# Kernel tuning notes

Hardware: AMD Instinct MI355X
Metric: run time of the kernel (lower is better)

Reference implementation:

```python
import jax, jax.numpy as jnp
import numpy as np

BSZ, T, D_IN, P, H, D_OUT = 8, 4096, 512, 256, 256, 512


def setup_inputs() -> dict:
    key = jax.random.key(0)
    ks = jax.random.split(key, 8)
    x_seq = jax.random.normal(ks[0], (BSZ, T, D_IN), dtype=jnp.float32)
    # stable diagonal transition: |a| < 1 so the 4096-step recurrence does not blow up
    a = jax.random.uniform(ks[1], (H,), minval=-0.99, maxval=0.99, dtype=jnp.float32)
    B = jax.random.normal(ks[2], (P, H), dtype=jnp.float32) * 0.05
    C = jax.random.normal(ks[3], (H, P), dtype=jnp.float32) * 0.05
    Wi = jax.random.normal(ks[4], (P, D_IN), dtype=jnp.float32) * 0.05
    bi = jax.random.normal(ks[5], (P,), dtype=jnp.float32) * 0.05
    Wo = jax.random.normal(ks[6], (D_OUT, P), dtype=jnp.float32) * 0.05
    bo = jax.random.normal(ks[7], (D_OUT,), dtype=jnp.float32) * 0.05
    return {"x_seq": x_seq, "a": a, "B": B, "C": C, "Wi": Wi, "bi": bi, "Wo": Wo, "bo": bo}


def reference(x_seq, a, B, C, Wi, bi, Wo, bo):
    # proj_in + relu (eqx.nn.Linear: y = W @ x + b), vmapped over batch and time
    x_proj = jax.nn.relu(jnp.einsum("btd,pd->btp", x_seq, Wi) + bi)  # [Bsz,T,P]
    # precompute driving input u_t = B^T x_t for every step
    u = jnp.einsum("btp,ph->bth", x_proj, B)  # [Bsz,T,H]
    u_t = jnp.swapaxes(u, 0, 1)  # [T,Bsz,H] (scan over time)

    def step(h, u_step):  # h: [Bsz,H]
        h = a * h + u_step
        return h, h

    h0 = jnp.zeros((x_seq.shape[0], a.shape[0]), dtype=x_seq.dtype)
    _, hs = jax.lax.scan(step, h0, u_t)  # hs: [T,Bsz,H]
    # y_t = C^T h_t, then proj_out
    y_seq = jnp.einsum("tbh,hp->btp", hs, C)  # [Bsz,T,P]
    y_out = jnp.einsum("btp,op->bto", y_seq, Wo) + bo  # [Bsz,T,D_out]
    return y_out
```

## Files before the change

kernel.cpp:

```cpp
#include <hip/hip_runtime.h>

#define BSZN 8
#define TT 4096
#define DIN 512
#define PP 256
#define HHH 256
#define DOUT 512
#define LCH 64
#define NCH (TT / LCH)
#define NBLK (BSZN * NCH)
#define XPS 264
#define AST 136

typedef __attribute__((ext_vector_type(8))) short bf16x8;
typedef __attribute__((ext_vector_type(4))) float f32x4;

#define GLOBAL_AS __attribute__((address_space(1)))
#define LDS_AS __attribute__((address_space(3)))

static __device__ __forceinline__ void gld_lds16(const void* g, void* l) {
  __builtin_amdgcn_global_load_lds((const GLOBAL_AS unsigned int*)g,
                                   (LDS_AS unsigned int*)l, 16, 0, 0);
}

static __device__ __forceinline__ unsigned short f2bf(float x) {
  union { float f; unsigned u; } t{x};
  unsigned r = t.u + 0x7fffu + ((t.u >> 16) & 1u);
  return (unsigned short)(r >> 16);
}

static __device__ __forceinline__ float ld_carry(const float* p) {
  return __hip_atomic_load(p, __ATOMIC_RELAXED, __HIP_MEMORY_SCOPE_AGENT);
}


__global__ __launch_bounds__(256) void prep_k(
    const float* __restrict__ Wi, const float* __restrict__ Wo,
    const float* __restrict__ Cm, const float* __restrict__ Bm,
    unsigned short* __restrict__ Wi_t, unsigned short* __restrict__ B_t,
    unsigned short* __restrict__ CWT_t, int* __restrict__ flag_g) {
  __shared__ alignas(16) char smem[8192];
  const int b = blockIdx.x, tid = threadIdx.x;
  if (b < 128) {
    const int idx = b * 1024 + tid * 4;
    const int row = idx >> 9, d = idx & 511;
    const float4 v = *(const float4*)(Wi + idx);
    uint2 w;
    w.x = (unsigned)f2bf(v.x) | ((unsigned)f2bf(v.y) << 16);
    w.y = (unsigned)f2bf(v.z) | ((unsigned)f2bf(v.w) << 16);
    const int tile = d >> 5, kc = (d >> 3) & 3, s = (kc + (row >> 1)) & 3;
    *(uint2*)(Wi_t + tile * 8192 + row * 32 + s * 8 + (d & 7)) = w;
  } else if (b < 144) {
    const int t = b - 128;
    const int p0 = (t >> 2) * 64, h0 = (t & 3) * 64;
#pragma unroll 4
    for (int it = 0; it < 16; ++it) {
      const int f = it * 256 + tid;
      const int h = h0 + (f >> 6), p = p0 + (f & 63);
      const unsigned short val = f2bf(Bm[(size_t)p * HHH + h]);
      const int tile = p >> 5, kc = (p >> 3) & 3, s = (kc + (h >> 1)) & 3;
      B_t[tile * 8192 + h * 32 + s * 8 + (p & 7)] = val;
    }
  } else if (b == 144) {
    flag_g[tid] = 0;
    flag_g[tid + 256] = 0;
  } else {
    const int t = b - 145;
    const int m0 = (t >> 2) * 64, n0 = (t & 3) * 64;
    char* As = smem;
    char* Bs = smem + 4096;
    const int wave = tid >> 6, lane = tid & 63;
    const int l15 = lane & 15, q = lane >> 4;
    const int wrow = (wave >> 1) * 32, wcol = (wave & 1) * 32;
    f32x4 acc[2][2];
#pragma unroll
    for (int i = 0; i < 2; ++i)
#pragma unroll
      for (int j = 0; j < 2; ++j) acc[i][j] = f32x4{0.f, 0.f, 0.f, 0.f};
    for (int k0 = 0; k0 < PP; k0 += 32) {
#pragma unroll
      for (int it = 0; it < 2; ++it) {
        const int f = it * 256 + tid;
        const int r = f >> 3, ck = (f & 7) * 4;
        float4 v = *(const float4*)(Wo + (size_t)(m0 + r) * PP + k0 + ck);
        uint2 w;
        w.x = (unsigned)f2bf(v.x) | ((unsigned)f2bf(v.y) << 16);
        w.y = (unsigned)f2bf(v.z) | ((unsigned)f2bf(v.w) << 16);
        *(uint2*)(As + r * 64 + ck * 2) = w;
        v = *(const float4*)(Cm + (size_t)(n0 + r) * PP + k0 + ck);
        w.x = (unsigned)f2bf(v.x) | ((unsigned)f2bf(v.y) << 16);
        w.y = (unsigned)f2bf(v.z) | ((unsigned)f2bf(v.w) << 16);
        *(uint2*)(Bs + r * 64 + ck * 2) = w;
      }
      __syncthreads();
      bf16x8 af[2], bfv[2];
#pragma unroll
      for (int mi = 0; mi < 2; ++mi)
        af[mi] = *(const bf16x8*)(As + (wrow + mi * 16 + l15) * 64 + q * 16);
#pragma unroll
      for (int ni = 0; ni < 2; ++ni)
        bfv[ni] = *(const bf16x8*)(Bs + (wcol + ni * 16 + l15) * 64 + q * 16);
#pragma unroll
      for (int mi = 0; mi < 2; ++mi)
#pragma unroll
        for (int ni = 0; ni < 2; ++ni)
          acc[mi][ni] = __builtin_amdgcn_mfma_f32_16x16x32_bf16(
              af[mi], bfv[ni], acc[mi][ni], 0, 0, 0);
      __syncthreads();
    }
#pragma unroll
    for (int mi = 0; mi < 2; ++mi)
#pragma unroll
      for (int ni = 0; ni < 2; ++ni)
#pragma unroll
        for (int reg = 0; reg < 4; ++reg) {
          const int row = m0 + wrow + mi * 16 + q * 4 + reg;
          const int col = n0 + wcol + ni * 16 + l15;
          const int tile = col >> 5, kc = (col >> 3) & 3;
          const int s = (kc + (row >> 1)) & 3;
          CWT_t[tile * 16384 + row * 32 + s * 8 + (col & 7)] =
              f2bf(acc[mi][ni][reg]);
        }
  }
}

__global__ __launch_bounds__(256, 2) void s4_mega(
    const float* __restrict__ x, const float* __restrict__ a,
    const unsigned short* __restrict__ Wi_t, const float* __restrict__ bi,
    const unsigned short* __restrict__ B_t,
    const unsigned short* __restrict__ CWT_t, const float* __restrict__ bo,
    float* __restrict__ out, float* __restrict__ carry_g,
    int* __restrict__ flag_g) {
  __shared__ alignas(16) char smem[67584];
  char* As = smem;
  unsigned short* xp = (unsigned short*)smem;
  char* TB0 = smem + 33792;
  char* TB1 = smem + 50176;
  float* PL = (float*)(smem + 66560);

  const int tid = threadIdx.x, wave = tid >> 6, lane = tid & 63;
  const int l15 = lane & 15, q = lane >> 4;
  const int bc = blockIdx.x, b = bc >> 6, c = bc & (NCH - 1);
  const size_t row0 = (size_t)bc * LCH;
  const int wc = wave * 64;

  int wrot[4];
#pragma unroll
  for (int ni = 0; ni < 4; ++ni) {
    const int r = wc + ni * 16 + l15;
    wrot[ni] = r * 64 + (((q + (r >> 1)) & 3) << 4);
  }
  int afb[4];
#pragma unroll
  for (int mi = 0; mi < 4; ++mi) afb[mi] = (mi * 16 + l15) * AST + q * 16;
  int xpb[4];
#pragma unroll
  for (int mi = 0; mi < 4; ++mi) xpb[mi] = (mi * 16 + l15) * XPS + q * 8;

  f32x4 acc[4][4];
#pragma unroll
  for (int i = 0; i < 4; ++i)
#pragma unroll
    for (int j = 0; j < 4; ++j) acc[i][j] = f32x4{0.f, 0.f, 0.f, 0.f};

  float4 xv[4];
#pragma unroll
  for (int i = 0; i < 4; ++i) {
    const int f = i * 256 + tid;
    xv[i] = *(const float4*)(x + (row0 + (f >> 4)) * DIN + (f & 15) * 4);
  }
  for (int t = 0; t < 8; ++t) {
    {
#pragma unroll
      for (int i = 0; i < 4; ++i) {
        const int f = i * 256 + tid;
        uint2 w;
        w.x = (unsigned)f2bf(xv[i].x) | ((unsigned)f2bf(xv[i].y) << 16);
        w.y = (unsigned)f2bf(xv[i].z) | ((unsigned)f2bf(xv[i].w) << 16);
        *(uint2*)(As + (f >> 4) * AST + (f & 15) * 8) = w;
      }
    }
    {
      const char* gw = (const char*)Wi_t + t * 32768 + wave * 4096 + lane * 16;
      char* l0 = TB0 + wave * 4096 + lane * 16;
      char* l1 = TB1 + wave * 4096 + lane * 16;
#pragma unroll
      for (int i = 0; i < 4; ++i) {
        gld_lds16(gw + i * 1024, l0 + i * 1024);
        gld_lds16(gw + 16384 + i * 1024, l1 + i * 1024);
      }
    }
    __syncthreads();
    if (t < 7) {
#pragma unroll
      for (int i = 0; i < 4; ++i) {
        const int f = i * 256 + tid;
        xv[i] = *(const float4*)(x + (row0 + (f >> 4)) * DIN + (t + 1) * 64 +
                                 (f & 15) * 4);
      }
    }
    bf16x8 af[4][2], bfv[4][2];
#pragma unroll
    for (int mi = 0; mi < 4; ++mi) {
      af[mi][0] = *(const bf16x8*)(As + afb[mi]);
      af[mi][1] = *(const bf16x8*)(As + afb[mi] + 64);
    }
#pragma unroll
    for (int ni = 0; ni < 4; ++ni) {
      bfv[ni][0] = *(const bf16x8*)(TB0 + wrot[ni]);
      bfv[ni][1] = *(const bf16x8*)(TB1 + wrot[ni]);
    }
#pragma unroll
    for (int kk = 0; kk < 2; ++kk)
#pragma unroll
      for (int mi = 0; mi < 4; ++mi)
#pragma unroll
        for (int ni = 0; ni < 4; ++ni)
          acc[mi][ni] = __builtin_amdgcn_mfma_f32_16x16x32_bf16(
              af[mi][kk], bfv[ni][kk], acc[mi][ni], 0, 0, 0);
    __syncthreads();
  }

#pragma unroll
  for (int ni = 0; ni < 4; ++ni) {
    const int col = wc + ni * 16 + l15;
    const float bb = bi[col];
#pragma unroll
    for (int mi = 0; mi < 4; ++mi)
#pragma unroll
      for (int reg = 0; reg < 4; ++reg) {
        const int row = mi * 16 + q * 4 + reg;
        xp[row * XPS + col] = f2bf(fmaxf(acc[mi][ni][reg] + bb, 0.f));
      }
  }
  __syncthreads();

#pragma unroll
  for (int i = 0; i < 4; ++i)
#pragma unroll
    for (int j = 0; j < 4; ++j) acc[i][j] = f32x4{0.f, 0.f, 0.f, 0.f};
  for (int t = 0; t < 4; ++t) {
    {
      const char* gw = (const char*)B_t + t * 32768 + wave * 4096 + lane * 16;
      char* l0 = TB0 + wave * 4096 + lane * 16;
      char* l1 = TB1 + wave * 4096 + lane * 16;
#pragma unroll
      for (int i = 0; i < 4; ++i) {
        gld_lds16(gw + i * 1024, l0 + i * 1024);
        gld_lds16(gw + 16384 + i * 1024, l1 + i * 1024);
      }
    }
    __syncthreads();
    bf16x8 af[4][2], bfv[4][2];
#pragma unroll
    for (int mi = 0; mi < 4; ++mi) {
      af[mi][0] = *(const bf16x8*)(xp + xpb[mi] + t * 64);
      af[mi][1] = *(const bf16x8*)(xp + xpb[mi] + t * 64 + 32);
    }
#pragma unroll
    for (int ni = 0; ni < 4; ++ni) {
      bfv[ni][0] = *(const bf16x8*)(TB0 + wrot[ni]);
      bfv[ni][1] = *(const bf16x8*)(TB1 + wrot[ni]);
    }
#pragma unroll
    for (int kk = 0; kk < 2; ++kk)
#pragma unroll
      for (int mi = 0; mi < 4; ++mi)
#pragma unroll
        for (int ni = 0; ni < 4; ++ni)
          acc[mi][ni] = __builtin_amdgcn_mfma_f32_16x16x32_bf16(
              af[mi][kk], bfv[ni][kk], acc[mi][ni], 0, 0, 0);
    __syncthreads();
  }

  float aC[4], Wz[4];
#pragma unroll
  for (int ni = 0; ni < 4; ++ni) aC[ni] = a[wc + ni * 16 + l15];
#pragma unroll
  for (int ni = 0; ni < 4; ++ni) {
    const float A = aC[ni];
    const float A2 = A * A, A4 = A2 * A2, A8 = A4 * A4, A16 = A8 * A8;
    const float A4q = ((q & 1) ? A4 : 1.f) * ((q & 2) ? A8 : 1.f);
    float W = 0.f;
#pragma unroll
    for (int mi = 0; mi < 4; ++mi) {
      f32x4 v = acc[mi][ni];
      v.y = fmaf(A, v.x, v.y);
      v.z = fmaf(A, v.y, v.z);
      v.w = fmaf(A, v.z, v.w);
      const float E = v.w;
      const float E0 = __shfl(E, l15, 64);
      const float E1 = __shfl(E, l15 + 16, 64);
      const float E2 = __shfl(E, l15 + 32, 64);
      const float E3 = __shfl(E, l15 + 48, 64);
      const float s1 = E0, s2 = fmaf(A4, s1, E1), s3 = fmaf(A4, s2, E2);
      const float s4 = fmaf(A4, s3, E3);
      const float Sq = (q == 0) ? 0.f : (q == 1) ? s1 : (q == 2) ? s2 : s3;
      const float sin_ = fmaf(A4q, W, Sq);
      v.x = fmaf(A, sin_, v.x);
      v.y = fmaf(A2, sin_, v.y);
      v.z = fmaf(A2 * A, sin_, v.z);
      v.w = fmaf(A4, sin_, v.w);
      acc[mi][ni] = v;
      W = fmaf(A16, W, s4);
    }
    Wz[ni] = W;
  }
  if (q == 0) {
#pragma unroll
    for (int ni = 0; ni < 4; ++ni)
      __hip_atomic_store(&carry_g[(size_t)bc * HHH + wc + ni * 16 + l15],
                         Wz[ni], __ATOMIC_RELAXED, __HIP_MEMORY_SCOPE_AGENT);
  }
  __syncthreads();
  if (tid == 0) {
    __threadfence();
    __hip_atomic_store(&flag_g[bc], 1, __ATOMIC_RELEASE,
                       __HIP_MEMORY_SCOPE_AGENT);
  }
  if (tid < c) {
    while (__hip_atomic_load(&flag_g[b * NCH + tid], __ATOMIC_ACQUIRE,
                             __HIP_MEMORY_SCOPE_AGENT) == 0)
      __builtin_amdgcn_s_sleep(8);
  }
  __syncthreads();
  {
    const int colp = tid;
    const float A = a[colp];
    float t1 = A;
#pragma unroll
    for (int j = 0; j < 6; ++j) t1 *= t1;
    const float A64 = t1, A128 = A64 * A64, A256 = A128 * A128;
    const float* cg = carry_g + (size_t)b * NCH * HHH + colp;
    float P = 0.f;
    int j = 0;
    for (; j + 4 <= c; j += 4) {
      const float c0 = ld_carry(cg + (size_t)j * HHH);
      const float c1 = ld_carry(cg + (size_t)(j + 1) * HHH);
      const float c2 = ld_carry(cg + (size_t)(j + 2) * HHH);
      const float c3 = ld_carry(cg + (size_t)(j + 3) * HHH);
      P = fmaf(A256, P, fmaf(A64, fmaf(A64, fmaf(A64, c0, c1), c2), c3));
    }
    for (; j < c; ++j) P = fmaf(A64, P, ld_carry(cg + (size_t)j * HHH));
    PL[colp] = P;
  }
  __syncthreads();
#pragma unroll
  for (int ni = 0; ni < 4; ++ni) {
    const float A = aC[ni];
    const float A2 = A * A, A4 = A2 * A2, A8 = A4 * A4, A16 = A8 * A8;
    const float A4q = ((q & 1) ? A4 : 1.f) * ((q & 2) ? A8 : 1.f);
    const float P = PL[wc + ni * 16 + l15];
    float fm = A4q * A * P;
#pragma unroll
    for (int mi = 0; mi < 4; ++mi) {
      f32x4 v = acc[mi][ni];
      v.x += fm;
      v.y = fmaf(A, fm, v.y);
      v.z = fmaf(A2, fm, v.z);
      v.w = fmaf(A2 * A, fm, v.w);
      acc[mi][ni] = v;
      fm *= A16;
    }
  }
  __syncthreads();

  unsigned short* hsL = (unsigned short*)smem;
#pragma unroll
  for (int ni = 0; ni < 4; ++ni) {
    const int col = wc + ni * 16 + l15;
#pragma unroll
    for (int mi = 0; mi < 4; ++mi)
#pragma unroll
      for (int reg = 0; reg < 4; ++reg)
        hsL[(mi * 16 + q * 4 + reg) * XPS + col] = f2bf(acc[mi][ni][reg]);
  }
  __syncthreads();

  int crot[2][4];
#pragma unroll
  for (int g = 0; g < 2; ++g)
#pragma unroll
    for (int ni = 0; ni < 4; ++ni) {
      const int r = wave * 128 + g * 64 + ni * 16 + l15;
      crot[g][ni] = r * 64 + (((q + (r >> 1)) & 3) << 4);
    }

  f32x4 oacc[2][4][4];
#pragma unroll
  for (int g = 0; g < 2; ++g)
#pragma unroll
    for (int i = 0; i < 4; ++i)
#pragma unroll
      for (int j = 0; j < 4; ++j) oacc[g][i][j] = f32x4{0.f, 0.f, 0.f, 0.f};
  for (int t = 0; t < 8; ++t) {
    {
      const char* gw =
          (const char*)CWT_t + t * 32768 + wave * 8192 + lane * 16;
      char* l0 = TB0 + wave * 8192 + lane * 16;
#pragma unroll
      for (int i = 0; i < 8; ++i) gld_lds16(gw + i * 1024, l0 + i * 1024);
    }
    __syncthreads();
    bf16x8 af[4], bfv[2][4];
#pragma unroll
    for (int mi = 0; mi < 4; ++mi)
      af[mi] = *(const bf16x8*)(hsL + xpb[mi] + t * 32);
#pragma unroll
    for (int g = 0; g < 2; ++g)
#pragma unroll
      for (int ni = 0; ni < 4; ++ni)
        bfv[g][ni] = *(const bf16x8*)(TB0 + crot[g][ni]);
#pragma unroll
    for (int g = 0; g < 2; ++g)
#pragma unroll
      for (int mi = 0; mi < 4; ++mi)
#pragma unroll
        for (int ni = 0; ni < 4; ++ni)
          oacc[g][mi][ni] = __builtin_amdgcn_mfma_f32_16x16x32_bf16(
              af[mi], bfv[g][ni], oacc[g][mi][ni], 0, 0, 0);
    __syncthreads();
  }
#pragma unroll
  for (int g = 0; g < 2; ++g)
#pragma unroll
    for (int ni = 0; ni < 4; ++ni) {
      const int ocol = wave * 128 + g * 64 + ni * 16 + l15;
      const float bb = bo[ocol];
#pragma unroll
      for (int mi = 0; mi < 4; ++mi)
#pragma unroll
        for (int reg = 0; reg < 4; ++reg) {
          const int row = mi * 16 + q * 4 + reg;
          out[(row0 + row) * DOUT + ocol] = oacc[g][mi][ni][reg] + bb;
        }
    }
}

extern "C" void kernel_launch(void* const* d_in, const int* in_sizes, int n_in,
                              void* d_out, int out_size, void* d_ws,
                              size_t ws_size, hipStream_t stream) {
  const float* x  = (const float*)d_in[0];
  const float* a  = (const float*)d_in[1];
  const float* Bm = (const float*)d_in[2];
  const float* Cm = (const float*)d_in[3];
  const float* Wi = (const float*)d_in[4];
  const float* bi = (const float*)d_in[5];
  const float* Wo = (const float*)d_in[6];
  const float* bo = (const float*)d_in[7];
  float* out = (float*)d_out;

  char* ws = (char*)d_ws;
  unsigned short* Wi_t  = (unsigned short*)ws; ws += (size_t)PP * DIN * 2;
  unsigned short* B_t   = (unsigned short*)ws; ws += (size_t)HHH * PP * 2;
  unsigned short* CWT_t = (unsigned short*)ws; ws += (size_t)DOUT * HHH * 2;
  float* carry_g = (float*)ws; ws += (size_t)NBLK * HHH * 4;
  int* flag_g = (int*)ws;

  prep_k<<<177, 256, 0, stream>>>(Wi, Wo, Cm, Bm, Wi_t, B_t, CWT_t, flag_g);
  s4_mega<<<NBLK, 256, 0, stream>>>(x, a, Wi_t, bi, B_t, CWT_t, bo, out,
                                    carry_g, flag_g);
}
```

Before: 188.7 us.

## Unfuse C and Wo into separate GEMMs and prefetch weight tiles early

The precomputed C·Wo product is dropped, so the prep kernel no longer runs a small GEMM and only converts and lays out B, C and Wo in parallel blocks. The main kernel now does an extra 64x256x256 GEMM with C before the Wo projection. The first weight tile of each stage is issued before the preceding epilogue to overlap its load, and a few barriers are removed. The carry-prefix loop is unrolled by 8 and the spin sleep is lengthened. This shortens the prep stage and hides load latency, at the cost of extra MFMA work per block and an extra bf16 rounding of the intermediate.

```diff
diff --git a/kernel.cpp b/kernel.cpp
--- a/kernel.cpp
+++ b/kernel.cpp
@@ -38,8 +38,8 @@
     const float* __restrict__ Wi, const float* __restrict__ Wo,
     const float* __restrict__ Cm, const float* __restrict__ Bm,
     unsigned short* __restrict__ Wi_t, unsigned short* __restrict__ B_t,
-    unsigned short* __restrict__ CWT_t, int* __restrict__ flag_g) {
-  __shared__ alignas(16) char smem[8192];
+    unsigned short* __restrict__ C_t, unsigned short* __restrict__ Wo_t,
+    int* __restrict__ flag_g) {
   const int b = blockIdx.x, tid = threadIdx.x;
   if (b < 128) {
     const int idx = b * 1024 + tid * 4;
@@ -50,77 +50,40 @@
     w.y = (unsigned)f2bf(v.z) | ((unsigned)f2bf(v.w) << 16);
     const int tile = d >> 5, kc = (d >> 3) & 3, s = (kc + (row >> 1)) & 3;
     *(uint2*)(Wi_t + tile * 8192 + row * 32 + s * 8 + (d & 7)) = w;
-  } else if (b < 144) {
-    const int t = b - 128;
-    const int p0 = (t >> 2) * 64, h0 = (t & 3) * 64;
-#pragma unroll 4
-    for (int it = 0; it < 16; ++it) {
-      const int f = it * 256 + tid;
-      const int h = h0 + (f >> 6), p = p0 + (f & 63);
-      const unsigned short val = f2bf(Bm[(size_t)p * HHH + h]);
-      const int tile = p >> 5, kc = (p >> 3) & 3, s = (kc + (h >> 1)) & 3;
-      B_t[tile * 8192 + h * 32 + s * 8 + (p & 7)] = val;
-    }
-  } else if (b == 144) {
+  } else if (b < 192) {
+    const int f = (b - 128) * 256 + tid;
+    const int p = f >> 6, h = (f & 63) * 4;
+    const float4 v = *(const float4*)(Bm + (size_t)p * HHH + h);
+    const float vv[4] = {v.x, v.y, v.z, v.w};
+    const int tile = p >> 5, kc = (p >> 3) & 3;
+#pragma unroll
+    for (int j = 0; j < 4; ++j) {
+      const int row = h + j, s = (kc + (row >> 1)) & 3;
+      B_t[tile * 8192 + row * 32 + s * 8 + (p & 7)] = f2bf(vv[j]);
+    }
+  } else if (b < 256) {
+    const int f = (b - 192) * 256 + tid;
+    const int h = f >> 6, p = (f & 63) * 4;
+    const float4 v = *(const float4*)(Cm + (size_t)h * PP + p);
+    const float vv[4] = {v.x, v.y, v.z, v.w};
+    const int tile = h >> 5, kc = (h >> 3) & 3;
+#pragma unroll
+    for (int j = 0; j < 4; ++j) {
+      const int row = p + j, s = (kc + (row >> 1)) & 3;
+      C_t[tile * 8192 + row * 32 + s * 8 + (h & 7)] = f2bf(vv[j]);
+    }
+  } else if (b < 384) {
+    const int idx = (b - 256) * 1024 + tid * 4;
+    const int o = idx >> 8, p = idx & 255;
+    const float4 v = *(const float4*)(Wo + idx);
+    uint2 w;
+    w.x = (unsigned)f2bf(v.x) | ((unsigned)f2bf(v.y) << 16);
+    w.y = (unsigned)f2bf(v.z) | ((unsigned)f2bf(v.w) << 16);
+    const int tile = p >> 5, kc = (p >> 3) & 3, s = (kc + (o >> 1)) & 3;
+    *(uint2*)(Wo_t + tile * 16384 + o * 32 + s * 8 + (p & 7)) = w;
+  } else {
     flag_g[tid] = 0;
     flag_g[tid + 256] = 0;
-  } else {
-    const int t = b - 145;
-    const int m0 = (t >> 2) * 64, n0 = (t & 3) * 64;
-    char* As = smem;
-    char* Bs = smem + 4096;
-    const int wave = tid >> 6, lane = tid & 63;
-    const int l15 = lane & 15, q = lane >> 4;
-    const int wrow = (wave >> 1) * 32, wcol = (wave & 1) * 32;
-    f32x4 acc[2][2];
-#pragma unroll
-    for (int i = 0; i < 2; ++i)
-#pragma unroll
-      for (int j = 0; j < 2; ++j) acc[i][j] = f32x4{0.f, 0.f, 0.f, 0.f};
-    for (int k0 = 0; k0 < PP; k0 += 32) {
-#pragma unroll
-      for (int it = 0; it < 2; ++it) {
-        const int f = it * 256 + tid;
-        const int r = f >> 3, ck = (f & 7) * 4;
-        float4 v = *(const float4*)(Wo + (size_t)(m0 + r) * PP + k0 + ck);
-        uint2 w;
-        w.x = (unsigned)f2bf(v.x) | ((unsigned)f2bf(v.y) << 16);
-        w.y = (unsigned)f2bf(v.z) | ((unsigned)f2bf(v.w) << 16);
-        *(uint2*)(As + r * 64 + ck * 2) = w;
-        v = *(const float4*)(Cm + (size_t)(n0 + r) * PP + k0 + ck);
-        w.x = (unsigned)f2bf(v.x) | ((unsigned)f2bf(v.y) << 16);
-        w.y = (unsigned)f2bf(v.z) | ((unsigned)f2bf(v.w) << 16);
-        *(uint2*)(Bs + r * 64 + ck * 2) = w;
-      }
-      __syncthreads();
-      bf16x8 af[2], bfv[2];
-#pragma unroll
-      for (int mi = 0; mi < 2; ++mi)
-        af[mi] = *(const bf16x8*)(As + (wrow + mi * 16 + l15) * 64 + q * 16);
-#pragma unroll
-      for (int ni = 0; ni < 2; ++ni)
-        bfv[ni] = *(const bf16x8*)(Bs + (wcol + ni * 16 + l15) * 64 + q * 16);
-#pragma unroll
-      for (int mi = 0; mi < 2; ++mi)
-#pragma unroll
-        for (int ni = 0; ni < 2; ++ni)
-          acc[mi][ni] = __builtin_amdgcn_mfma_f32_16x16x32_bf16(
-              af[mi], bfv[ni], acc[mi][ni], 0, 0, 0);
-      __syncthreads();
-    }
-#pragma unroll
-    for (int mi = 0; mi < 2; ++mi)
-#pragma unroll
-      for (int ni = 0; ni < 2; ++ni)
-#pragma unroll
-        for (int reg = 0; reg < 4; ++reg) {
-          const int row = m0 + wrow + mi * 16 + q * 4 + reg;
-          const int col = n0 + wcol + ni * 16 + l15;
-          const int tile = col >> 5, kc = (col >> 3) & 3;
-          const int s = (kc + (row >> 1)) & 3;
-          CWT_t[tile * 16384 + row * 32 + s * 8 + (col & 7)] =
-              f2bf(acc[mi][ni][reg]);
-        }
   }
 }
 
@@ -128,14 +91,14 @@
     const float* __restrict__ x, const float* __restrict__ a,
     const unsigned short* __restrict__ Wi_t, const float* __restrict__ bi,
     const unsigned short* __restrict__ B_t,
-    const unsigned short* __restrict__ CWT_t, const float* __restrict__ bo,
+    const unsigned short* __restrict__ C_t,
+    const unsigned short* __restrict__ Wo_t, const float* __restrict__ bo,
     float* __restrict__ out, float* __restrict__ carry_g,
     int* __restrict__ flag_g) {
   __shared__ alignas(16) char smem[67584];
   char* As = smem;
   unsigned short* xp = (unsigned short*)smem;
-  char* TB0 = smem + 33792;
-  char* TB1 = smem + 50176;
+  char* TB = smem + 33792;
   float* PL = (float*)(smem + 66560);
 
   const int tid = threadIdx.x, wave = tid >> 6, lane = tid & 63;
@@ -150,12 +113,22 @@
     const int r = wc + ni * 16 + l15;
     wrot[ni] = r * 64 + (((q + (r >> 1)) & 3) << 4);
   }
+  int crot[2][4];
+#pragma unroll
+  for (int g = 0; g < 2; ++g)
+#pragma unroll
+    for (int ni = 0; ni < 4; ++ni) {
+      const int r = wave * 128 + g * 64 + ni * 16 + l15;
+      crot[g][ni] = r * 64 + (((q + (r >> 1)) & 3) << 4);
+    }
   int afb[4];
 #pragma unroll
   for (int mi = 0; mi < 4; ++mi) afb[mi] = (mi * 16 + l15) * AST + q * 16;
   int xpb[4];
 #pragma unroll
   for (int mi = 0; mi < 4; ++mi) xpb[mi] = (mi * 16 + l15) * XPS + q * 8;
+
+  const int sbase = wave * 4096 + lane * 16;
 
   f32x4 acc[4][4];
 #pragma unroll
@@ -170,24 +143,20 @@
     xv[i] = *(const float4*)(x + (row0 + (f >> 4)) * DIN + (f & 15) * 4);
   }
   for (int t = 0; t < 8; ++t) {
+#pragma unroll
+    for (int i = 0; i < 4; ++i) {
+      const int f = i * 256 + tid;
+      uint2 w;
+      w.x = (unsigned)f2bf(xv[i].x) | ((unsigned)f2bf(xv[i].y) << 16);
+      w.y = (unsigned)f2bf(xv[i].z) | ((unsigned)f2bf(xv[i].w) << 16);
+      *(uint2*)(As + (f >> 4) * AST + (f & 15) * 8) = w;
+    }
     {
+      const char* gw = (const char*)Wi_t + t * 32768 + sbase;
 #pragma unroll
       for (int i = 0; i < 4; ++i) {
-        const int f = i * 256 + tid;
-        uint2 w;
-        w.x = (unsigned)f2bf(xv[i].x) | ((unsigned)f2bf(xv[i].y) << 16);
-        w.y = (unsigned)f2bf(xv[i].z) | ((unsigned)f2bf(xv[i].w) << 16);
-        *(uint2*)(As + (f >> 4) * AST + (f & 15) * 8) = w;
-      }
-    }
-    {
-      const char* gw = (const char*)Wi_t + t * 32768 + wave * 4096 + lane * 16;
-      char* l0 = TB0 + wave * 4096 + lane * 16;
-      char* l1 = TB1 + wave * 4096 + lane * 16;
-#pragma unroll
-      for (int i = 0; i < 4; ++i) {
-        gld_lds16(gw + i * 1024, l0 + i * 1024);
-        gld_lds16(gw + 16384 + i * 1024, l1 + i * 1024);
+        gld_lds16(gw + i * 1024, TB + sbase + i * 1024);
+        gld_lds16(gw + 16384 + i * 1024, TB + 16384 + sbase + i * 1024);
       }
     }
     __syncthreads();
@@ -207,8 +176,8 @@
     }
 #pragma unroll
     for (int ni = 0; ni < 4; ++ni) {
-      bfv[ni][0] = *(const bf16x8*)(TB0 + wrot[ni]);
-      bfv[ni][1] = *(const bf16x8*)(TB1 + wrot[ni]);
+      bfv[ni][0] = *(const bf16x8*)(TB + wrot[ni]);
+      bfv[ni][1] = *(const bf16x8*)(TB + 16384 + wrot[ni]);
     }
 #pragma unroll
     for (int kk = 0; kk < 2; ++kk)
@@ -219,6 +188,15 @@
           acc[mi][ni] = __builtin_amdgcn_mfma_f32_16x16x32_bf16(
               af[mi][kk], bfv[ni][kk], acc[mi][ni], 0, 0, 0);
     __syncthreads();
+  }
+
+  {
+    const char* gw = (const char*)B_t + sbase;
+#pragma unroll
+    for (int i = 0; i < 4; ++i) {
+      gld_lds16(gw + i * 1024, TB + sbase + i * 1024);
+      gld_lds16(gw + 16384 + i * 1024, TB + 16384 + sbase + i * 1024);
+    }
   }
 
 #pragma unroll
@@ -233,21 +211,18 @@
         xp[row * XPS + col] = f2bf(fmaxf(acc[mi][ni][reg] + bb, 0.f));
       }
   }
-  __syncthreads();
 
 #pragma unroll
   for (int i = 0; i < 4; ++i)
 #pragma unroll
     for (int j = 0; j < 4; ++j) acc[i][j] = f32x4{0.f, 0.f, 0.f, 0.f};
   for (int t = 0; t < 4; ++t) {
-    {
-      const char* gw = (const char*)B_t + t * 32768 + wave * 4096 + lane * 16;
-      char* l0 = TB0 + wave * 4096 + lane * 16;
-      char* l1 = TB1 + wave * 4096 + lane * 16;
+    if (t > 0) {
+      const char* gw = (const char*)B_t + t * 32768 + sbase;
 #pragma unroll
       for (int i = 0; i < 4; ++i) {
-        gld_lds16(gw + i * 1024, l0 + i * 1024);
-        gld_lds16(gw + 16384 + i * 1024, l1 + i * 1024);
+        gld_lds16(gw + i * 1024, TB + sbase + i * 1024);
+        gld_lds16(gw + 16384 + i * 1024, TB + 16384 + sbase + i * 1024);
       }
     }
     __syncthreads();
@@ -259,8 +234,8 @@
     }
 #pragma unroll
     for (int ni = 0; ni < 4; ++ni) {
-      bfv[ni][0] = *(const bf16x8*)(TB0 + wrot[ni]);
-      bfv[ni][1] = *(const bf16x8*)(TB1 + wrot[ni]);
+      bfv[ni][0] = *(const bf16x8*)(TB + wrot[ni]);
+      bfv[ni][1] = *(const bf16x8*)(TB + 16384 + wrot[ni]);
     }
 #pragma unroll
     for (int kk = 0; kk < 2; ++kk)
@@ -318,10 +293,18 @@
     __hip_atomic_store(&flag_g[bc], 1, __ATOMIC_RELEASE,
                        __HIP_MEMORY_SCOPE_AGENT);
   }
+  {
+    const char* gw = (const char*)C_t + sbase;
+#pragma unroll
+    for (int i = 0; i < 4; ++i) {
+      gld_lds16(gw + i * 1024, TB + sbase + i * 1024);
+      gld_lds16(gw + 16384 + i * 1024, TB + 16384 + sbase + i * 1024);
+    }
+  }
   if (tid < c) {
     while (__hip_atomic_load(&flag_g[b * NCH + tid], __ATOMIC_ACQUIRE,
                              __HIP_MEMORY_SCOPE_AGENT) == 0)
-      __builtin_amdgcn_s_sleep(8);
+      __builtin_amdgcn_s_sleep(32);
   }
   __syncthreads();
   {
@@ -331,15 +314,18 @@
 #pragma unroll
     for (int j = 0; j < 6; ++j) t1 *= t1;
     const float A64 = t1, A128 = A64 * A64, A256 = A128 * A128;
+    const float A512 = A256 * A256;
     const float* cg = carry_g + (size_t)b * NCH * HHH + colp;
     float P = 0.f;
     int j = 0;
-    for (; j + 4 <= c; j += 4) {
-      const float c0 = ld_carry(cg + (size_t)j * HHH);
-      const float c1 = ld_carry(cg + (size_t)(j + 1) * HHH);
-      const float c2 = ld_carry(cg + (size_t)(j + 2) * HHH);
-      const float c3 = ld_carry(cg + (size_t)(j + 3) * HHH);
-      P = fmaf(A256, P, fmaf(A64, fmaf(A64, fmaf(A64, c0, c1), c2), c3));
+    for (; j + 8 <= c; j += 8) {
+      float cv[8];
+#pragma unroll
+      for (int i = 0; i < 8; ++i) cv[i] = ld_carry(cg + (size_t)(j + i) * HHH);
+      float u = cv[0];
+#pragma unroll
+      for (int i = 1; i < 8; ++i) u = fmaf(A64, u, cv[i]);
+      P = fmaf(A512, P, u);
     }
     for (; j < c; ++j) P = fmaf(A64, P, ld_carry(cg + (size_t)j * HHH));
     PL[colp] = P;
@@ -375,16 +361,57 @@
       for (int reg = 0; reg < 4; ++reg)
         hsL[(mi * 16 + q * 4 + reg) * XPS + col] = f2bf(acc[mi][ni][reg]);
   }
-  __syncthreads();
-
-  int crot[2][4];
-#pragma unroll
-  for (int g = 0; g < 2; ++g)
+#pragma unroll
+  for (int i = 0; i < 4; ++i)
+#pragma unroll
+    for (int j = 0; j < 4; ++j) acc[i][j] = f32x4{0.f, 0.f, 0.f, 0.f};
+  for (int t = 0; t < 4; ++t) {
+    if (t > 0) {
+      const char* gw = (const char*)C_t + t * 32768 + sbase;
+#pragma unroll
+      for (int i = 0; i < 4; ++i) {
+        gld_lds16(gw + i * 1024, TB + sbase + i * 1024);
+        gld_lds16(gw + 16384 + i * 1024, TB + 16384 + sbase + i * 1024);
+      }
+    }
+    __syncthreads();
+    bf16x8 af[4][2], bfv[4][2];
+#pragma unroll
+    for (int mi = 0; mi < 4; ++mi) {
+      af[mi][0] = *(const bf16x8*)(hsL + xpb[mi] + t * 64);
+      af[mi][1] = *(const bf16x8*)(hsL + xpb[mi] + t * 64 + 32);
+    }
 #pragma unroll
     for (int ni = 0; ni < 4; ++ni) {
-      const int r = wave * 128 + g * 64 + ni * 16 + l15;
-      crot[g][ni] = r * 64 + (((q + (r >> 1)) & 3) << 4);
-    }
+      bfv[ni][0] = *(const bf16x8*)(TB + wrot[ni]);
+      bfv[ni][1] = *(const bf16x8*)(TB + 16384 + wrot[ni]);
+    }
+#pragma unroll
+    for (int kk = 0; kk < 2; ++kk)
+#pragma unroll
+      for (int mi = 0; mi < 4; ++mi)
+#pragma unroll
+        for (int ni = 0; ni < 4; ++ni)
+          acc[mi][ni] = __builtin_amdgcn_mfma_f32_16x16x32_bf16(
+              af[mi][kk], bfv[ni][kk], acc[mi][ni], 0, 0, 0);
+    __syncthreads();
+  }
+
+  {
+    const char* gw = (const char*)Wo_t + wave * 8192 + lane * 16;
+#pragma unroll
+    for (int i = 0; i < 8; ++i)
+      gld_lds16(gw + i * 1024, TB + wave * 8192 + lane * 16 + i * 1024);
+  }
+#pragma unroll
+  for (int ni = 0; ni < 4; ++ni) {
+    const int col = wc + ni * 16 + l15;
+#pragma unroll
+    for (int mi = 0; mi < 4; ++mi)
+#pragma unroll
+      for (int reg = 0; reg < 4; ++reg)
+        hsL[(mi * 16 + q * 4 + reg) * XPS + col] = f2bf(acc[mi][ni][reg]);
+  }
 
   f32x4 oacc[2][4][4];
 #pragma unroll
@@ -394,12 +421,11 @@
 #pragma unroll
       for (int j = 0; j < 4; ++j) oacc[g][i][j] = f32x4{0.f, 0.f, 0.f, 0.f};
   for (int t = 0; t < 8; ++t) {
-    {
-      const char* gw =
-          (const char*)CWT_t + t * 32768 + wave * 8192 + lane * 16;
-      char* l0 = TB0 + wave * 8192 + lane * 16;
-#pragma unroll
-      for (int i = 0; i < 8; ++i) gld_lds16(gw + i * 1024, l0 + i * 1024);
+    if (t > 0) {
+      const char* gw = (const char*)Wo_t + t * 32768 + wave * 8192 + lane * 16;
+#pragma unroll
+      for (int i = 0; i < 8; ++i)
+        gld_lds16(gw + i * 1024, TB + wave * 8192 + lane * 16 + i * 1024);
     }
     __syncthreads();
     bf16x8 af[4], bfv[2][4];
@@ -410,7 +436,7 @@
     for (int g = 0; g < 2; ++g)
 #pragma unroll
       for (int ni = 0; ni < 4; ++ni)
-        bfv[g][ni] = *(const bf16x8*)(TB0 + crot[g][ni]);
+        bfv[g][ni] = *(const bf16x8*)(TB + crot[g][ni]);
 #pragma unroll
     for (int g = 0; g < 2; ++g)
 #pragma unroll
@@ -451,13 +477,15 @@
   float* out = (float*)d_out;
 
   char* ws = (char*)d_ws;
-  unsigned short* Wi_t  = (unsigned short*)ws; ws += (size_t)PP * DIN * 2;
-  unsigned short* B_t   = (unsigned short*)ws; ws += (size_t)HHH * PP * 2;
-  unsigned short* CWT_t = (unsigned short*)ws; ws += (size_t)DOUT * HHH * 2;
+  unsigned short* Wi_t = (unsigned short*)ws; ws += (size_t)PP * DIN * 2;
+  unsigned short* B_t  = (unsigned short*)ws; ws += (size_t)HHH * PP * 2;
+  unsigned short* C_t  = (unsigned short*)ws; ws += (size_t)HHH * PP * 2;
+  unsigned short* Wo_t = (unsigned short*)ws; ws += (size_t)DOUT * PP * 2;
   float* carry_g = (float*)ws; ws += (size_t)NBLK * HHH * 4;
   int* flag_g = (int*)ws;
 
-  prep_k<<<177, 256, 0, stream>>>(Wi, Wo, Cm, Bm, Wi_t, B_t, CWT_t, flag_g);
-  s4_mega<<<NBLK, 256, 0, stream>>>(x, a, Wi_t, bi, B_t, CWT_t, bo, out,
+  prep_k<<<385, 256, 0, stream>>>(Wi, Wo, Cm, Bm, Wi_t, B_t, C_t, Wo_t,
+                                  flag_g);
+  s4_mega<<<NBLK, 256, 0, stream>>>(x, a, Wi_t, bi, B_t, C_t, Wo_t, bo, out,
                                     carry_g, flag_g);
 }
```

Result: no change. 189.7 us (+0.5%).
